# Performance work log

Hardware: AMD Instinct MI355X
Metric: run time of the kernel (lower is better)

## Reference

```python
import jax, jax.numpy as jnp
import numpy as np
import math

NC = 80              # num classes
NA = 18              # 3 anchor shapes x 6 angles
NCH = 5 + 1 + NC     # x,y,w,h,a,conf,cls...
STRIDES = [8, 16]
SXY = [1.2, 1.1]
ANCH = [[[10, 13], [16, 30], [33, 23]], [[30, 61], [62, 45], [59, 119]]]
RAD = math.pi / 180.0
ANGLES = [RAD * a for a in (-60.0, -30.0, 0.0, 30.0, 60.0, 90.0)]


def _masked_anchors(level):
    s = STRIDES[level]
    return jnp.array([[w / s, h / s, a] for (w, h) in ANCH[level] for a in ANGLES],
                     dtype=jnp.float32)  # [18, 3]


def _decode(feat, W, b, level):
    # feat: [B, C, G, G], W: [out_ch, C], b: [out_ch]
    B, C, G, _ = feat.shape
    out = jnp.einsum('bchw,oc->bohw', feat, W) + b[None, :, None, None]  # 1x1 conv
    pred = out.reshape(B, NA, NCH, G, G).transpose(0, 1, 3, 4, 2)  # [B, A, gy, gx, NCH]
    sxy = SXY[level]
    s = float(STRIDES[level])
    ma = _masked_anchors(level)
    aw = ma[:, 0][None, :, None, None]
    ah = ma[:, 1][None, :, None, None]
    aa = ma[:, 2][None, :, None, None]
    gx = jnp.arange(G, dtype=pred.dtype)[None, None, None, :]
    gy = jnp.arange(G, dtype=pred.dtype)[None, None, :, None]
    px = jax.nn.sigmoid(pred[..., 0]) * sxy - (sxy - 1.0) / 2.0 + gx
    py = jax.nn.sigmoid(pred[..., 1]) * sxy - (sxy - 1.0) / 2.0 + gy
    pw = jnp.exp(pred[..., 2]) * aw
    ph = jnp.exp(pred[..., 3]) * ah
    pa = pred[..., 4] + aa
    conf = jax.nn.sigmoid(pred[..., 5])
    cls = jax.nn.sigmoid(pred[..., 6:])
    boxes = jnp.stack([px * s, py * s, pw * s, ph * s, pa], axis=-1)  # xywh scaled, angle raw
    out = jnp.concatenate([boxes, conf[..., None], cls], axis=-1)
    return out.reshape(B, -1, NCH)


def setup_inputs() -> dict:
    key = jax.random.key(0)
    k = jax.random.split(key, 6)
    return {
        'x0': jax.random.normal(k[0], (8, 256, 64, 64), dtype=jnp.float32),
        'x1': jax.random.normal(k[1], (8, 512, 32, 32), dtype=jnp.float32),
        'W0': jax.random.normal(k[2], (1548, 256), dtype=jnp.float32) * 0.02,
        'b0': jnp.zeros((1548,), dtype=jnp.float32),
        'W1': jax.random.normal(k[3], (1548, 512), dtype=jnp.float32) * 0.02,
        'b1': jnp.zeros((1548,), dtype=jnp.float32),
    }


def reference(x0, x1, W0, b0, W1, b1):
    o0 = _decode(x0, W0, b0, 0)  # [B, 18*64*64, 86]
    o1 = _decode(x1, W1, b1, 1)  # [B, 18*32*32, 86]
    return jnp.concatenate([o0, o1], axis=1)
```

## Files before the change

kernel.cpp:

```cpp
#include <hip/hip_runtime.h>
#include <hip/hip_bf16.h>


typedef __attribute__((ext_vector_type(8))) short short8;
typedef __attribute__((ext_vector_type(4))) short short4v;
typedef __attribute__((ext_vector_type(4))) float f32x4;
typedef unsigned int u32;

__device__ __forceinline__ unsigned short f2bf(float f) {
    union { float f; unsigned u; } c; c.f = f;
    return (unsigned short)((c.u + 0x7fffu + ((c.u >> 16) & 1u)) >> 16);
}
__device__ __forceinline__ float sigm(float v) {
    return 1.0f / (1.0f + __expf(-v));
}
__device__ __forceinline__ void gload16(const void* g, void* l) {
    __builtin_amdgcn_global_load_lds(
        (const __attribute__((address_space(1))) u32*)g,
        (__attribute__((address_space(3))) u32*)l, 16, 0, 0);
}

#define OUT_CH 1548
#define NCHN   86
#define BPB    7925760


__global__ void conv_w_kernel(const float* __restrict__ W0, unsigned short* __restrict__ Wb0,
                              const float* __restrict__ W1, unsigned short* __restrict__ Wb1) {
    int i = blockIdx.x * blockDim.x + threadIdx.x;
    if (i >= 297216) return;
    const float* W = W0;
    unsigned short* Wb = Wb0;
    if (i >= 99072) { W = W1; Wb = Wb1; i -= 99072; }
    const float4 f = ((const float4*)W)[i];
    short4v v;
    v[0] = (short)f2bf(f.x); v[1] = (short)f2bf(f.y);
    v[2] = (short)f2bf(f.z); v[3] = (short)f2bf(f.w);
    ((short4v*)Wb)[i] = v;
}

__global__ void transpose_x_kernel(const float* __restrict__ X, unsigned short* __restrict__ Xb,
                                   int C, int GG) {
    __shared__ float sT[64][65];
    const int p0 = blockIdx.x * 64;
    const int c0 = blockIdx.y * 64;
    const int b  = blockIdx.z;
    const int tid = threadIdx.x;
    const float* src = X + ((size_t)b * C + c0) * GG + p0;
    const int rc = tid >> 4;
    const int cp = (tid & 15) * 4;
    #pragma unroll
    for (int rr = 0; rr < 4; ++rr) {
        const int c = rc + rr * 16;
        const float4 f = *(const float4*)&src[(size_t)c * GG + cp];
        sT[c][cp + 0] = f.x; sT[c][cp + 1] = f.y;
        sT[c][cp + 2] = f.z; sT[c][cp + 3] = f.w;
    }
    __syncthreads();
    const int p  = tid >> 2;
    const int cg = (tid & 3) * 16;
    unsigned short u[16];
    #pragma unroll
    for (int k = 0; k < 16; ++k) u[k] = f2bf(sT[cg + k][p]);
    unsigned short* dst = Xb + ((size_t)b * GG + p0 + p) * C + c0 + cg;
    *(short8*)dst       = *(const short8*)&u[0];
    *(short8*)(dst + 8) = *(const short8*)&u[8];
}


__global__ __launch_bounds__(256, 4) void detect_gemm(
    const unsigned short* __restrict__ Xb0, const unsigned short* __restrict__ Xb1,
    const unsigned short* __restrict__ Wb0, const unsigned short* __restrict__ Wb1,
    const float* __restrict__ b0, const float* __restrict__ b1,
    float* __restrict__ out)
{
    __shared__ __attribute__((aligned(128))) char smem[40960];
    unsigned short* sAbase = (unsigned short*)smem;
    unsigned short* sBbase = (unsigned short*)(smem + 16384);
    float* sOutF = (float*)smem;

    const int bid = blockIdx.x;
    const int v   = (bid & 7) * 1440 + (bid >> 3);
    const int mt  = v / 18;
    const int a   = v - mt * 18;

    const bool lvl1 = (mt >= 512);
    const unsigned short* __restrict__ Xb = lvl1 ? Xb1 : Xb0;
    const unsigned short* __restrict__ Wb = lvl1 ? Wb1 : Wb0;
    const float* __restrict__ biasA = (lvl1 ? b1 : b0) + a * NCHN;
    const int C   = lvl1 ? 512 : 256;
    const int GG  = lvl1 ? 1024 : 4096;
    const int Gsh = lvl1 ? 5 : 6;
    const float sxy     = lvl1 ? 1.1f : 1.2f;
    const float sxy_off = (sxy - 1.0f) * 0.5f;
    const float sf      = lvl1 ? 16.0f : 8.0f;
    const int shp  = a / 6;
    const int angi = a - shp * 6;
    const float aw = lvl1 ? ((shp == 0) ? 30.f : (shp == 1) ? 62.f : 59.f)
                          : ((shp == 0) ? 10.f : (shp == 1) ? 16.f : 33.f);
    const float ah = lvl1 ? ((shp == 0) ? 61.f : (shp == 1) ? 45.f : 119.f)
                          : ((shp == 0) ? 13.f : (shp == 1) ? 30.f : 23.f);
    const float aa = (angi == 0) ? -1.04719755119659775f :
                     (angi == 1) ? -0.52359877559829887f :
                     (angi == 2) ?  0.0f :
                     (angi == 3) ?  0.52359877559829887f :
                     (angi == 4) ?  1.04719755119659775f :
                                    1.57079632679489662f;

    const int tloc = lvl1 ? (mt - 512) : mt;
    const int b  = tloc >> (lvl1 ? 4 : 6);
    const int p0 = (tloc & ((lvl1 ? 16 : 64) - 1)) * 64;

    const unsigned short* __restrict__ Xp = Xb + ((size_t)b * GG + p0) * C;

    const int tid  = threadIdx.x;
    const int lane = tid & 63;
    const int wid  = tid >> 6;
    const int wm = wid >> 1;
    const int wn = wid & 1;

    f32x4 acc[2][3];
    #pragma unroll
    for (int i = 0; i < 2; ++i)
        #pragma unroll
        for (int j = 0; j < 3; ++j)
            acc[i][j] = f32x4{0.f, 0.f, 0.f, 0.f};

    const int rowIn = lane >> 3;
    const int scolE = ((((lane & 7) << 4)) ^ (rowIn << 4)) >> 1;

    const int lr   = lane & 15;
    const int kqb  = (lane >> 4) << 4;
    const int swzR = (lr & 7) << 4;

    const int KT = C >> 6;

    auto stage = [&](int bufsel, int kt) {
        const int k0 = kt << 6;
        unsigned short* sA = sAbase + bufsel * 4096;
        unsigned short* sB = sBbase + bufsel * 6144;
        #pragma unroll
        for (int i = 0; i < 2; ++i) {
            const int c = i * 4 + wid;
            const int row = c * 8 + rowIn;
            gload16(Xp + (size_t)row * C + k0 + scolE, (char*)sA + (c << 10));
        }
        #pragma unroll
        for (int j = 0; j < 3; ++j) {
            const int c = j * 4 + wid;
            const int row = c * 8 + rowIn;
            int grow = a * NCHN + row;
            grow = grow > (OUT_CH - 1) ? (OUT_CH - 1) : grow;
            gload16(Wb + (size_t)grow * C + k0 + scolE, (char*)sB + (c << 10));
        }
    };

    auto compute = [&](int bufsel) {
        const char* sA = (const char*)(sAbase + bufsel * 4096);
        const char* sB = (const char*)(sBbase + bufsel * 6144);
        #pragma unroll
        for (int kk = 0; kk < 2; ++kk) {
            const int cb = (kk << 6) + kqb;
            short8 af[2], bfr[3];
            #pragma unroll
            for (int i = 0; i < 2; ++i) {
                const int ra = wm * 32 + i * 16 + lr;
                af[i] = *(const short8*)(sA + ra * 128 + (cb ^ swzR));
            }
            #pragma unroll
            for (int j = 0; j < 3; ++j) {
                const int rb = wn * 48 + j * 16 + lr;
                bfr[j] = *(const short8*)(sB + rb * 128 + (cb ^ swzR));
            }
            #pragma unroll
            for (int i = 0; i < 2; ++i)
                #pragma unroll
                for (int j = 0; j < 3; ++j)
                    acc[i][j] = __builtin_amdgcn_mfma_f32_16x16x32_bf16(af[i], bfr[j], acc[i][j], 0, 0, 0);
        }
    };

    stage(0, 0);
    __syncthreads();
    int cur = 0;
    for (int kt = 0; kt < KT; ++kt) {
        if (kt + 1 < KT) stage(cur ^ 1, kt + 1);
        compute(cur);
        __syncthreads();
        cur ^= 1;
    }

    const int rq = (lane >> 4) * 4;
    const int lvloff = lvl1 ? 73728 : 0;

    #pragma unroll
    for (int j = 0; j < 3; ++j) {
        const int ch = wn * 48 + j * 16 + lr;
        if (ch < NCHN) {
            const float bv = biasA[ch];
            #pragma unroll
            for (int i = 0; i < 2; ++i) {
                #pragma unroll
                for (int r = 0; r < 4; ++r) {
                    const int px = wm * 32 + i * 16 + rq + r;
                    const int p  = p0 + px;
                    const float vv = acc[i][j][r] + bv;
                    float res;
                    if (ch == 0)      res = (sigm(vv) * sxy - sxy_off + (float)(p & ((1 << Gsh) - 1))) * sf;
                    else if (ch == 1) res = (sigm(vv) * sxy - sxy_off + (float)(p >> Gsh)) * sf;
                    else if (ch == 2) res = __expf(vv) * aw;
                    else if (ch == 3) res = __expf(vv) * ah;
                    else if (ch == 4) res = vv + aa;
                    else              res = sigm(vv);
                    sOutF[px * NCHN + ch] = res;
                }
            }
        }
    }
    __syncthreads();

    const size_t spanDw = (size_t)b * BPB + ((size_t)(lvloff + a * GG + p0)) * NCHN;
    #pragma unroll
    for (int k = 0; k < 6; ++k) {
        const int f4 = tid + k * 256;
        if (f4 < 1376) {
            const f32x4 vv = *(const f32x4*)&sOutF[f4 * 4];
            __builtin_nontemporal_store(vv, (f32x4*)&out[spanDw + f4 * 4]);
        }
    }
}

extern "C" void kernel_launch(void* const* d_in, const int* in_sizes, int n_in,
                              void* d_out, int out_size, void* d_ws, size_t ws_size,
                              hipStream_t stream) {
    const float* x0 = (const float*)d_in[0];
    const float* x1 = (const float*)d_in[1];
    const float* W0 = (const float*)d_in[2];
    const float* b0 = (const float*)d_in[3];
    const float* W1 = (const float*)d_in[4];
    const float* b1 = (const float*)d_in[5];
    float* out = (float*)d_out;

    constexpr size_t XB0_OFF = 0;
    constexpr size_t XB1_OFF = 16777216;
    constexpr size_t WB0_OFF = 25165824;
    constexpr size_t WB1_OFF = 25958400;

    unsigned short* Xb0 = (unsigned short*)((char*)d_ws + XB0_OFF);
    unsigned short* Xb1 = (unsigned short*)((char*)d_ws + XB1_OFF);
    unsigned short* Wb0 = (unsigned short*)((char*)d_ws + WB0_OFF);
    unsigned short* Wb1 = (unsigned short*)((char*)d_ws + WB1_OFF);

    hipLaunchKernelGGL(conv_w_kernel, dim3((297216 + 255) / 256), dim3(256), 0, stream,
                       W0, Wb0, W1, Wb1);
    hipLaunchKernelGGL(transpose_x_kernel, dim3(64, 4, 8), dim3(256), 0, stream,
                       x0, Xb0, 256, 4096);
    hipLaunchKernelGGL(transpose_x_kernel, dim3(16, 8, 8), dim3(256), 0, stream,
                       x1, Xb1, 512, 1024);

    hipLaunchKernelGGL(detect_gemm, dim3(11520), dim3(256), 0, stream,
                       Xb0, Xb1, Wb0, Wb1, b0, b1, out);
}
```

Measured before the change: 148.6 us.

## Load A fragments directly to registers and stage full-K B tile in LDS

Replaces the double-buffered 64-wide K pipeline with a single stage. A operands are now read straight from global memory into registers as MFMA fragments, and the whole 256-wide K slice of B is staged into LDS at once, with a second pass only for level 1. This removes most per-iteration barriers and the LDS round trip for A. In exchange it uses more registers and LDS, lowers the launch-bounds occupancy hint from 4 to 3, and loses overlap between loads and compute inside a block.

```diff
diff --git a/kernel.cpp b/kernel.cpp
--- a/kernel.cpp
+++ b/kernel.cpp
@@ -68,15 +68,13 @@
 }
 
 
-__global__ __launch_bounds__(256, 4) void detect_gemm(
+__global__ __launch_bounds__(256, 3) void detect_gemm(
     const unsigned short* __restrict__ Xb0, const unsigned short* __restrict__ Xb1,
     const unsigned short* __restrict__ Wb0, const unsigned short* __restrict__ Wb1,
     const float* __restrict__ b0, const float* __restrict__ b1,
     float* __restrict__ out)
 {
-    __shared__ __attribute__((aligned(128))) char smem[40960];
-    unsigned short* sAbase = (unsigned short*)smem;
-    unsigned short* sBbase = (unsigned short*)(smem + 16384);
+    __shared__ __attribute__((aligned(128))) char smem[49152];
     float* sOutF = (float*)smem;
 
     const int bid = blockIdx.x;
@@ -111,8 +109,6 @@
     const int b  = tloc >> (lvl1 ? 4 : 6);
     const int p0 = (tloc & ((lvl1 ? 16 : 64) - 1)) * 64;
 
-    const unsigned short* __restrict__ Xp = Xb + ((size_t)b * GG + p0) * C;
-
     const int tid  = threadIdx.x;
     const int lane = tid & 63;
     const int wid  = tid >> 6;
@@ -132,63 +128,65 @@
     const int lr   = lane & 15;
     const int kqb  = (lane >> 4) << 4;
     const int swzR = (lr & 7) << 4;
-
-    const int KT = C >> 6;
-
-    auto stage = [&](int bufsel, int kt) {
-        const int k0 = kt << 6;
-        unsigned short* sA = sAbase + bufsel * 4096;
-        unsigned short* sB = sBbase + bufsel * 6144;
-        #pragma unroll
-        for (int i = 0; i < 2; ++i) {
-            const int c = i * 4 + wid;
-            const int row = c * 8 + rowIn;
-            gload16(Xp + (size_t)row * C + k0 + scolE, (char*)sA + (c << 10));
-        }
-        #pragma unroll
-        for (int j = 0; j < 3; ++j) {
-            const int c = j * 4 + wid;
-            const int row = c * 8 + rowIn;
-            int grow = a * NCHN + row;
-            grow = grow > (OUT_CH - 1) ? (OUT_CH - 1) : grow;
-            gload16(Wb + (size_t)grow * C + k0 + scolE, (char*)sB + (c << 10));
+    const int kb16 = kqb;
+
+    auto stageB = [&](int k0) {
+        #pragma unroll
+        for (int s = 0; s < 4; ++s) {
+            #pragma unroll
+            for (int j = 0; j < 3; ++j) {
+                const int c = j * 4 + wid;
+                const int row = c * 8 + rowIn;
+                int grow = a * NCHN + row;
+                grow = grow > (OUT_CH - 1) ? (OUT_CH - 1) : grow;
+                gload16(Wb + (size_t)grow * C + k0 + s * 64 + scolE,
+                        smem + s * 12288 + (c << 10));
+            }
         }
     };
 
-    auto compute = [&](int bufsel) {
-        const char* sA = (const char*)(sAbase + bufsel * 4096);
-        const char* sB = (const char*)(sBbase + bufsel * 6144);
-        #pragma unroll
-        for (int kk = 0; kk < 2; ++kk) {
-            const int cb = (kk << 6) + kqb;
-            short8 af[2], bfr[3];
-            #pragma unroll
-            for (int i = 0; i < 2; ++i) {
-                const int ra = wm * 32 + i * 16 + lr;
-                af[i] = *(const short8*)(sA + ra * 128 + (cb ^ swzR));
-            }
+    const char* ApBase = (const char*)(Xb + ((size_t)b * GG + p0 + wm * 32 + lr) * C);
+    const size_t Arow16 = (size_t)16 * C * 2;
+    short8 a8[2][8];
+    auto loadA = [&](int k0) {
+        #pragma unroll
+        for (int i = 0; i < 2; ++i)
+            #pragma unroll
+            for (int kk = 0; kk < 8; ++kk)
+                a8[i][kk] = *(const short8*)(ApBase + i * Arow16 + (size_t)k0 * 2 + kk * 64 + kb16);
+    };
+
+    auto computeHalf = [&]() {
+        #pragma unroll
+        for (int kk = 0; kk < 8; ++kk) {
+            const int s  = kk >> 1;
+            const int cb = ((kk & 1) << 6) + kqb;
+            short8 bfr[3];
             #pragma unroll
             for (int j = 0; j < 3; ++j) {
                 const int rb = wn * 48 + j * 16 + lr;
-                bfr[j] = *(const short8*)(sB + rb * 128 + (cb ^ swzR));
+                bfr[j] = *(const short8*)(smem + s * 12288 + rb * 128 + (cb ^ swzR));
             }
             #pragma unroll
             for (int i = 0; i < 2; ++i)
                 #pragma unroll
                 for (int j = 0; j < 3; ++j)
-                    acc[i][j] = __builtin_amdgcn_mfma_f32_16x16x32_bf16(af[i], bfr[j], acc[i][j], 0, 0, 0);
+                    acc[i][j] = __builtin_amdgcn_mfma_f32_16x16x32_bf16(a8[i][kk], bfr[j], acc[i][j], 0, 0, 0);
         }
     };
 
-    stage(0, 0);
-    __syncthreads();
-    int cur = 0;
-    for (int kt = 0; kt < KT; ++kt) {
-        if (kt + 1 < KT) stage(cur ^ 1, kt + 1);
-        compute(cur);
+    loadA(0);
+    stageB(0);
+    __syncthreads();
+    computeHalf();
+    if (lvl1) {
         __syncthreads();
-        cur ^= 1;
-    }
+        loadA(256);
+        stageB(256);
+        __syncthreads();
+        computeHalf();
+    }
+    __syncthreads();
 
     const int rq = (lane >> 4) * 4;
     const int lvloff = lvl1 ? 73728 : 0;
```

After: 247.9 us. 66.8% more time.

## Keep X tile resident in LDS and loop over nine anchors per block

Applied to the files above, without the earlier changes.

Each block now loads its whole X pixel tile (128 or 64 pixels by the full channel depth) into LDS once, then streams weight slices for nine anchors through a double buffer, running a fused epilogue and store after each anchor. The grid shrinks from 11520 small blocks to 768 blocks of 512 threads using about 142 KB of LDS. This cuts the repeated global loads of X across anchors and the per-block launch overhead. The cost is one block per CU, fewer blocks than before to spread across the GPU, and store and epilogue work serialised within each block.

```diff
diff --git a/kernel.cpp b/kernel.cpp
--- a/kernel.cpp
+++ b/kernel.cpp
@@ -68,50 +68,41 @@
 }
 
 
-__global__ __launch_bounds__(256, 4) void detect_gemm(
+__global__ __launch_bounds__(512, 1) void detect_gemm(
     const unsigned short* __restrict__ Xb0, const unsigned short* __restrict__ Xb1,
     const unsigned short* __restrict__ Wb0, const unsigned short* __restrict__ Wb1,
     const float* __restrict__ b0, const float* __restrict__ b1,
     float* __restrict__ out)
 {
-    __shared__ __attribute__((aligned(128))) char smem[40960];
-    unsigned short* sAbase = (unsigned short*)smem;
-    unsigned short* sBbase = (unsigned short*)(smem + 16384);
-    float* sOutF = (float*)smem;
+    __shared__ __attribute__((aligned(128))) char smem[145472];
+    float* sOutF = (float*)(smem + 98304);
+    float* sBias = (float*)(smem + 142336);
 
     const int bid = blockIdx.x;
-    const int v   = (bid & 7) * 1440 + (bid >> 3);
-    const int mt  = v / 18;
-    const int a   = v - mt * 18;
-
-    const bool lvl1 = (mt >= 512);
+    const int v   = (bid & 7) * 96 + (bid >> 3);
+    const bool lvl1 = (v >= 512);
+
+    int b, p0, grp;
+    if (!lvl1) { const int m = v >> 1;        grp = v & 1;  b = m >> 5; p0 = (m & 31) * 128; }
+    else       { const int u = (v - 512) >> 1; grp = v & 1; b = u >> 4; p0 = (u & 15) * 64; }
+    const int aBase = grp * 9;
+
     const unsigned short* __restrict__ Xb = lvl1 ? Xb1 : Xb0;
     const unsigned short* __restrict__ Wb = lvl1 ? Wb1 : Wb0;
-    const float* __restrict__ biasA = (lvl1 ? b1 : b0) + a * NCHN;
-    const int C   = lvl1 ? 512 : 256;
-    const int GG  = lvl1 ? 1024 : 4096;
-    const int Gsh = lvl1 ? 5 : 6;
+    const float* __restrict__ bias = lvl1 ? b1 : b0;
+    const int C     = lvl1 ? 512 : 256;
+    const int GG    = lvl1 ? 1024 : 4096;
+    const int Gsh   = lvl1 ? 5 : 6;
+    const int KT    = lvl1 ? 8 : 4;
+    const int ktsh  = lvl1 ? 3 : 2;
+    const int ktMask= KT - 1;
+    const int pitch = C * 2;
+    const int MI    = lvl1 ? 1 : 2;
+    const int MROWS = lvl1 ? 16 : 32;
     const float sxy     = lvl1 ? 1.1f : 1.2f;
     const float sxy_off = (sxy - 1.0f) * 0.5f;
     const float sf      = lvl1 ? 16.0f : 8.0f;
-    const int shp  = a / 6;
-    const int angi = a - shp * 6;
-    const float aw = lvl1 ? ((shp == 0) ? 30.f : (shp == 1) ? 62.f : 59.f)
-                          : ((shp == 0) ? 10.f : (shp == 1) ? 16.f : 33.f);
-    const float ah = lvl1 ? ((shp == 0) ? 61.f : (shp == 1) ? 45.f : 119.f)
-                          : ((shp == 0) ? 13.f : (shp == 1) ? 30.f : 23.f);
-    const float aa = (angi == 0) ? -1.04719755119659775f :
-                     (angi == 1) ? -0.52359877559829887f :
-                     (angi == 2) ?  0.0f :
-                     (angi == 3) ?  0.52359877559829887f :
-                     (angi == 4) ?  1.04719755119659775f :
-                                    1.57079632679489662f;
-
-    const int tloc = lvl1 ? (mt - 512) : mt;
-    const int b  = tloc >> (lvl1 ? 4 : 6);
-    const int p0 = (tloc & ((lvl1 ? 16 : 64) - 1)) * 64;
-
-    const unsigned short* __restrict__ Xp = Xb + ((size_t)b * GG + p0) * C;
+    const int lvloff    = lvl1 ? 73728 : 0;
 
     const int tid  = threadIdx.x;
     const int lane = tid & 63;
@@ -119,6 +110,12 @@
     const int wm = wid >> 1;
     const int wn = wid & 1;
 
+    #pragma unroll
+    for (int k = 0; k < 2; ++k) {
+        const int idx = tid + k * 512;
+        if (idx < 9 * NCHN) sBias[idx] = bias[aBase * NCHN + idx];
+    }
+
     f32x4 acc[2][3];
     #pragma unroll
     for (int i = 0; i < 2; ++i)
@@ -126,107 +123,147 @@
         for (int j = 0; j < 3; ++j)
             acc[i][j] = f32x4{0.f, 0.f, 0.f, 0.f};
 
-    const int rowIn = lane >> 3;
-    const int scolE = ((((lane & 7) << 4)) ^ (rowIn << 4)) >> 1;
+    const int rowAin = lvl1 ? (tid >> 6) : (tid >> 5);
+    const int colbA  = (lvl1 ? (tid & 63) : (tid & 31)) << 4;
+    const int scolAe = (colbA ^ ((rowAin & 7) << 4)) >> 1;
+    const int rpiA   = lvl1 ? 8 : 16;
+    const unsigned short* __restrict__ Xp = Xb + ((size_t)b * GG + p0) * C;
+
+    const int rowInB = lane >> 3;
+    const int scolBe = (((lane & 7) << 4) ^ (rowInB << 4)) >> 1;
 
     const int lr   = lane & 15;
     const int kqb  = (lane >> 4) << 4;
     const int swzR = (lr & 7) << 4;
 
-    const int KT = C >> 6;
-
-    auto stage = [&](int bufsel, int kt) {
+    int rowAb[2], rowBb[3];
+    #pragma unroll
+    for (int i = 0; i < 2; ++i) rowAb[i] = (wm * MROWS + i * 16 + lr) * pitch;
+    #pragma unroll
+    for (int j = 0; j < 3; ++j) rowBb[j] = (wn * 48 + j * 16 + lr) * 128;
+
+    auto stageB = [&](int s) {
+        const int aL = s >> ktsh;
+        const int kt = s & ktMask;
         const int k0 = kt << 6;
-        unsigned short* sA = sAbase + bufsel * 4096;
-        unsigned short* sB = sBbase + bufsel * 6144;
-        #pragma unroll
-        for (int i = 0; i < 2; ++i) {
-            const int c = i * 4 + wid;
-            const int row = c * 8 + rowIn;
-            gload16(Xp + (size_t)row * C + k0 + scolE, (char*)sA + (c << 10));
-        }
-        #pragma unroll
-        for (int j = 0; j < 3; ++j) {
-            const int c = j * 4 + wid;
-            const int row = c * 8 + rowIn;
-            int grow = a * NCHN + row;
+        const int ag = aBase + aL;
+        char* dst = smem + 65536 + (s & 1) * 16384;
+        #pragma unroll
+        for (int j = 0; j < 2; ++j) {
+            const int c = j * 8 + wid;
+            const int row = c * 8 + rowInB;
+            int grow = ag * NCHN + row;
             grow = grow > (OUT_CH - 1) ? (OUT_CH - 1) : grow;
-            gload16(Wb + (size_t)grow * C + k0 + scolE, (char*)sB + (c << 10));
+            gload16(Wb + (size_t)grow * C + k0 + scolBe, dst + (c << 10));
         }
     };
 
-    auto compute = [&](int bufsel) {
-        const char* sA = (const char*)(sAbase + bufsel * 4096);
-        const char* sB = (const char*)(sBbase + bufsel * 6144);
+    auto compute = [&](int s) {
+        const char* bb = smem + 65536 + (s & 1) * 16384;
+        const int kt = s & ktMask;
         #pragma unroll
         for (int kk = 0; kk < 2; ++kk) {
-            const int cb = (kk << 6) + kqb;
+            const int ca  = ((kt << 7) + (kk << 6) + kqb) ^ swzR;
+            const int cbB = ((kk << 6) + kqb) ^ swzR;
             short8 af[2], bfr[3];
             #pragma unroll
-            for (int i = 0; i < 2; ++i) {
-                const int ra = wm * 32 + i * 16 + lr;
-                af[i] = *(const short8*)(sA + ra * 128 + (cb ^ swzR));
-            }
+            for (int i = 0; i < 2; ++i)
+                if (i < MI) af[i] = *(const short8*)(smem + rowAb[i] + ca);
             #pragma unroll
-            for (int j = 0; j < 3; ++j) {
-                const int rb = wn * 48 + j * 16 + lr;
-                bfr[j] = *(const short8*)(sB + rb * 128 + (cb ^ swzR));
-            }
+            for (int j = 0; j < 3; ++j)
+                bfr[j] = *(const short8*)(bb + rowBb[j] + cbB);
             #pragma unroll
             for (int i = 0; i < 2; ++i)
+                if (i < MI)
+                    #pragma unroll
+                    for (int j = 0; j < 3; ++j)
+                        acc[i][j] = __builtin_amdgcn_mfma_f32_16x16x32_bf16(af[i], bfr[j], acc[i][j], 0, 0, 0);
+        }
+    };
+
+    const int rq = (lane >> 4) * 4;
+    const int nf4 = lvl1 ? 1376 : 2752;
+
+    auto epilogue = [&](int aL) {
+        const int ag = aBase + aL;
+        const int shp  = ag / 6;
+        const int angi = ag - shp * 6;
+        const float aw = lvl1 ? ((shp == 0) ? 30.f : (shp == 1) ? 62.f : 59.f)
+                              : ((shp == 0) ? 10.f : (shp == 1) ? 16.f : 33.f);
+        const float ah = lvl1 ? ((shp == 0) ? 61.f : (shp == 1) ? 45.f : 119.f)
+                              : ((shp == 0) ? 13.f : (shp == 1) ? 30.f : 23.f);
+        const float aa = (angi == 0) ? -1.04719755119659775f :
+                         (angi == 1) ? -0.52359877559829887f :
+                         (angi == 2) ?  0.0f :
+                         (angi == 3) ?  0.52359877559829887f :
+                         (angi == 4) ?  1.04719755119659775f :
+                                        1.57079632679489662f;
+        #pragma unroll
+        for (int j = 0; j < 3; ++j) {
+            const int ch = wn * 48 + j * 16 + lr;
+            if (ch < NCHN) {
+                const float bv = sBias[aL * NCHN + ch];
                 #pragma unroll
-                for (int j = 0; j < 3; ++j)
-                    acc[i][j] = __builtin_amdgcn_mfma_f32_16x16x32_bf16(af[i], bfr[j], acc[i][j], 0, 0, 0);
-        }
-    };
-
-    stage(0, 0);
-    __syncthreads();
-    int cur = 0;
-    for (int kt = 0; kt < KT; ++kt) {
-        if (kt + 1 < KT) stage(cur ^ 1, kt + 1);
-        compute(cur);
-        __syncthreads();
-        cur ^= 1;
-    }
-
-    const int rq = (lane >> 4) * 4;
-    const int lvloff = lvl1 ? 73728 : 0;
-
-    #pragma unroll
-    for (int j = 0; j < 3; ++j) {
-        const int ch = wn * 48 + j * 16 + lr;
-        if (ch < NCHN) {
-            const float bv = biasA[ch];
-            #pragma unroll
-            for (int i = 0; i < 2; ++i) {
-                #pragma unroll
-                for (int r = 0; r < 4; ++r) {
-                    const int px = wm * 32 + i * 16 + rq + r;
-                    const int p  = p0 + px;
-                    const float vv = acc[i][j][r] + bv;
-                    float res;
-                    if (ch == 0)      res = (sigm(vv) * sxy - sxy_off + (float)(p & ((1 << Gsh) - 1))) * sf;
-                    else if (ch == 1) res = (sigm(vv) * sxy - sxy_off + (float)(p >> Gsh)) * sf;
-                    else if (ch == 2) res = __expf(vv) * aw;
-                    else if (ch == 3) res = __expf(vv) * ah;
-                    else if (ch == 4) res = vv + aa;
-                    else              res = sigm(vv);
-                    sOutF[px * NCHN + ch] = res;
+                for (int i = 0; i < 2; ++i) {
+                    if (i >= MI) continue;
+                    #pragma unroll
+                    for (int r = 0; r < 4; ++r) {
+                        const int px = wm * MROWS + i * 16 + rq + r;
+                        const int p  = p0 + px;
+                        const float vv = acc[i][j][r] + bv;
+                        float res;
+                        if (ch == 0)      res = (sigm(vv) * sxy - sxy_off + (float)(p & ((1 << Gsh) - 1))) * sf;
+                        else if (ch == 1) res = (sigm(vv) * sxy - sxy_off + (float)(p >> Gsh)) * sf;
+                        else if (ch == 2) res = __expf(vv) * aw;
+                        else if (ch == 3) res = __expf(vv) * ah;
+                        else if (ch == 4) res = vv + aa;
+                        else              res = sigm(vv);
+                        sOutF[px * NCHN + ch] = res;
+                    }
                 }
             }
         }
-    }
-    __syncthreads();
-
-    const size_t spanDw = (size_t)b * BPB + ((size_t)(lvloff + a * GG + p0)) * NCHN;
-    #pragma unroll
-    for (int k = 0; k < 6; ++k) {
-        const int f4 = tid + k * 256;
-        if (f4 < 1376) {
-            const f32x4 vv = *(const f32x4*)&sOutF[f4 * 4];
-            __builtin_nontemporal_store(vv, (f32x4*)&out[spanDw + f4 * 4]);
-        }
+        asm volatile("s_waitcnt lgkmcnt(0)" ::: "memory");
+        __builtin_amdgcn_s_barrier();
+        const size_t span = (size_t)b * BPB + ((size_t)(lvloff + ag * GG + p0)) * NCHN;
+        #pragma unroll
+        for (int k = 0; k < 6; ++k) {
+            const int f4 = tid + k * 512;
+            if (f4 < nf4) {
+                const f32x4 vv = *(const f32x4*)&sOutF[f4 * 4];
+                __builtin_nontemporal_store(vv, (f32x4*)&out[span + (size_t)f4 * 4]);
+            }
+        }
+        asm volatile("s_waitcnt vmcnt(2)" ::: "memory");
+        __builtin_amdgcn_s_barrier();
+        #pragma unroll
+        for (int i = 0; i < 2; ++i)
+            #pragma unroll
+            for (int j = 0; j < 3; ++j)
+                acc[i][j] = f32x4{0.f, 0.f, 0.f, 0.f};
+    };
+
+    #pragma unroll
+    for (int i = 0; i < 8; ++i)
+        gload16(Xp + (size_t)(i * rpiA + rowAin) * C + scolAe, smem + i * 8192 + tid * 16);
+    stageB(0);
+    stageB(1);
+    asm volatile("s_waitcnt lgkmcnt(0)" ::: "memory");
+    asm volatile("s_waitcnt vmcnt(2)" ::: "memory");
+    __builtin_amdgcn_s_barrier();
+
+    const int S = 9 << ktsh;
+    for (int s = 0; s < S; ++s) {
+        compute(s);
+        __builtin_amdgcn_s_barrier();
+        if (s + 2 < S) {
+            stageB(s + 2);
+            asm volatile("s_waitcnt vmcnt(2)" ::: "memory");
+        } else {
+            asm volatile("s_waitcnt vmcnt(0)" ::: "memory");
+        }
+        __builtin_amdgcn_s_barrier();
+        if ((s & ktMask) == ktMask) epilogue(s >> ktsh);
     }
 }
 
@@ -258,6 +295,6 @@
     hipLaunchKernelGGL(transpose_x_kernel, dim3(16, 8, 8), dim3(256), 0, stream,
                        x1, Xb1, 512, 1024);
 
-    hipLaunchKernelGGL(detect_gemm, dim3(11520), dim3(256), 0, stream,
+    hipLaunchKernelGGL(detect_gemm, dim3(768), dim3(512), 0, stream,
                        Xb0, Xb1, Wb0, Wb1, b0, b1, out);
 }
```

After: 186.4 us. +25.4%, slower.
